# Kernel tuning notes

Measured on AMD Instinct MI355X. Metric: run time of the kernel, lower is better.

The kernel has to match this reference:

```python
import jax, jax.numpy as jnp
import numpy as np

N, M, IN_DIM, OUT_DIM = 32768, 8192, 256, 64


def setup_inputs() -> dict:
    key = jax.random.key(0)
    k1, k2, k3, k4 = jax.random.split(key, 4)
    H = jax.random.bernoulli(k1, 0.01, (N, M)).astype(jnp.float32)
    w = jax.random.uniform(k2, (M,), minval=0.5, maxval=1.5, dtype=jnp.float32)
    x = jax.random.normal(k3, (N, IN_DIM), dtype=jnp.float32)
    W_lin = jax.random.normal(k4, (IN_DIM, OUT_DIM), dtype=jnp.float32) * (1.0 / np.sqrt(IN_DIM))
    b_lin = jnp.zeros((OUT_DIM,), dtype=jnp.float32)
    return {"x": x, "H": H, "w": w, "W_lin": W_lin, "b_lin": b_lin}


def reference(x, H, w, W_lin, b_lin):
    # Theta = Dv^{-1/2} H diag(w) De^{-1} H^T Dv^{-1/2}; out = Theta @ (x W + b).
    # Applied right-to-left with O(N) diagonal broadcasts instead of materializing
    # the [N, N] operator -- identical math to the torch reference.
    De = jnp.clip(jnp.sum(H, axis=0), 1.0, None)                 # [M] edge degrees
    Dv = jnp.clip(jnp.sum(H * w[None, :], axis=1), 1e-6, None)   # [N] weighted node degrees
    dv_inv_sqrt = Dv ** -0.5                                     # [N]
    y = x @ W_lin + b_lin                                        # [N, out]
    t = H.T @ (dv_inv_sqrt[:, None] * y)                         # [M, out] gather to edges
    t = (w / De)[:, None] * t                                    # edge scaling W De^{-1}
    out = dv_inv_sqrt[:, None] * (H @ t)                         # [N, out] scatter back
    return out
```

## Files before the change

### kernel.cpp

```cpp
#include <hip/hip_runtime.h>

#define N_NODES 32768
#define M_EDGES 8192
#define IN_DIM  256
#define OUT_F   64

#define KC1 16
#define KC2 4

#define NB8 (N_NODES / 8)
#define MB8 (M_EDGES / 8)

typedef __attribute__((ext_vector_type(8))) short  bf16x8;
typedef __attribute__((ext_vector_type(4))) float  f32x4;

__device__ __forceinline__ unsigned short f2bf_rne(float f) {
    unsigned u = __float_as_uint(f);
    unsigned r = (u + 0x7FFFu + ((u >> 16) & 1u)) >> 16;
    return (unsigned short)r;
}
__device__ __forceinline__ float bf2f(unsigned short h) {
    return __uint_as_float(((unsigned)h) << 16);
}


__global__ __launch_bounds__(256) void k_pack(const float* __restrict__ H,
                                              unsigned char* __restrict__ Hb) {
    int lane = threadIdx.x & 63;
    int wv   = threadIdx.x >> 6;
    int n = blockIdx.x * 4 + wv;
    const float4* Hrow = (const float4*)(H + (size_t)n * M_EDGES);
    unsigned* hb_row = (unsigned*)(Hb + (size_t)n * MB8);

    for (int i0 = 0; i0 < 32; i0 += 4) {
        float4 h0 = Hrow[(i0 + 0) * 64 + lane];
        float4 h1 = Hrow[(i0 + 1) * 64 + lane];
        float4 h2 = Hrow[(i0 + 2) * 64 + lane];
        float4 h3 = Hrow[(i0 + 3) * 64 + lane];
        #define PACK1(hv, ii)                                                  \
        {                                                                      \
            unsigned long long B0 = __ballot(hv.x != 0.f);                     \
            unsigned long long B1 = __ballot(hv.y != 0.f);                     \
            unsigned long long B2 = __ballot(hv.z != 0.f);                     \
            unsigned long long B3 = __ballot(hv.w != 0.f);                     \
            unsigned long long s01 = (lane & 2) ? B1 : B0;                     \
            unsigned long long s23 = (lane & 2) ? B3 : B2;                     \
            unsigned long long ss  = (lane & 4) ? s23 : s01;                   \
            unsigned v = (lane & 1) ? (unsigned)(ss >> 32) : (unsigned)ss;     \
            if (lane < 8) hb_row[(ii) * 8 + lane] = v;                         \
        }
        PACK1(h0, i0 + 0)
        PACK1(h1, i0 + 1)
        PACK1(h2, i0 + 2)
        PACK1(h3, i0 + 3)
        #undef PACK1
    }
}

__global__ __launch_bounds__(256) void k_bt(const unsigned char* __restrict__ Hb,
                                            unsigned char* __restrict__ HTb) {
    int lane = threadIdx.x & 63;
    int wv   = threadIdx.x >> 6;
    int id = blockIdx.x * 4 + wv;
    int D  = id & 255;
    int n0 = (id >> 8) * 64;
    unsigned u = *(const unsigned*)(Hb + (size_t)(n0 + lane) * MB8 + D * 4);
    int mbase = ((D >> 3) << 8) + ((D & 1) << 7) + ((D >> 1) & 3);
    unsigned long long acc = 0;
    #pragma unroll
    for (int b = 0; b < 32; ++b) {
        unsigned long long bal = __ballot((u >> b) & 1u);
        acc = (lane == b) ? bal : acc;
    }
    if (lane < 32)
        *(unsigned long long*)(HTb + (size_t)(mbase + 4 * lane) * NB8 + (n0 >> 3)) = acc;
}

__global__ __launch_bounds__(256) void k_dv(const unsigned char* __restrict__ Hb,
                                            const float* __restrict__ w,
                                            float* __restrict__ Dv_raw) {
    int lane = threadIdx.x & 63;
    int wv   = threadIdx.x >> 6;
    int n = blockIdx.x * 4 + wv;
    const uint4* row = (const uint4*)(Hb + (size_t)n * MB8);
    uint4 u4 = row[lane];
    float dv = 0.f;
    #define DVD(uu, dd)                                                        \
    {                                                                          \
        unsigned u = (uu);                                                     \
        int D = lane * 4 + (dd);                                               \
        int base = ((D >> 3) << 8) + ((D & 1) << 7) + ((D >> 1) & 3);          \
        while (u) { int p = __ffs(u) - 1; dv += w[base + 4 * p]; u &= u - 1; } \
    }
    DVD(u4.x, 0) DVD(u4.y, 1) DVD(u4.z, 2) DVD(u4.w, 3)
    #undef DVD
    for (int off = 32; off; off >>= 1) dv += __shfl_down(dv, off, 64);
    if (lane == 0) Dv_raw[n] = dv;
}

__global__ __launch_bounds__(256) void k_lin(const float* __restrict__ x,
                                             const float* __restrict__ Wl,
                                             const float* __restrict__ b,
                                             float* __restrict__ y) {
    __shared__ float x_s[16 * IN_DIM];
    int tid = threadIdx.x;
    int n0 = blockIdx.x * 16;
    for (int i = tid; i < 16 * IN_DIM / 4; i += 256)
        ((float4*)x_s)[i] = ((const float4*)(x + (size_t)n0 * IN_DIM))[i];
    __syncthreads();
    int k = tid & 63;
    int rbase = tid >> 6;
    for (int pass = 0; pass < 4; ++pass) {
        int r = pass * 4 + rbase;
        float acc = b[k];
        const float* xr = x_s + r * IN_DIM;
        #pragma unroll 8
        for (int i = 0; i < IN_DIM; ++i)
            acc = fmaf(xr[i], Wl[i * OUT_F + k], acc);
        y[(size_t)(n0 + r) * OUT_F + k] = acc;
    }
}

__global__ __launch_bounds__(256) void k_zt(const float* __restrict__ y,
                                            const float* __restrict__ Dv_raw,
                                            unsigned short* __restrict__ zTh,
                                            unsigned short* __restrict__ zTl) {
    __shared__ unsigned short zh_s[64][264];
    __shared__ unsigned short zl_s[64][264];
    __shared__ float dvis_s[256];
    int t = threadIdx.x;
    int n0 = blockIdx.x * 256;
    dvis_s[t] = rsqrtf(fmaxf(Dv_raw[n0 + t], 1e-6f));
    __syncthreads();
    int c = t & 15, rp = t >> 4;
    for (int it = 0; it < 16; ++it) {
        int r = it * 16 + rp;
        float4 v = ((const float4*)(y + (size_t)(n0 + r) * OUT_F))[c];
        float dvs = dvis_s[r];
        float zv[4] = { v.x * dvs, v.y * dvs, v.z * dvs, v.w * dvs };
        #pragma unroll
        for (int j = 0; j < 4; ++j) {
            unsigned short hi = f2bf_rne(zv[j]);
            float lo = zv[j] - bf2f(hi);
            zh_s[4 * c + j][r] = hi;
            zl_s[4 * c + j][r] = f2bf_rne(lo);
        }
    }
    __syncthreads();
    int lane = t & 63, wv = t >> 6;
    for (int i = 0; i < 16; ++i) {
        int kk = wv * 16 + i;
        *(ushort4*)(zTh + (size_t)kk * N_NODES + n0 + lane * 4) =
            *(const ushort4*)&zh_s[kk][lane * 4];
        *(ushort4*)(zTl + (size_t)kk * N_NODES + n0 + lane * 4) =
            *(const ushort4*)&zl_s[kk][lane * 4];
    }
}

__global__ __launch_bounds__(256) void g1(const unsigned char* __restrict__ HTb,
                                          const unsigned short* __restrict__ zTh,
                                          const unsigned short* __restrict__ zTl,
                                          float* __restrict__ t_part) {
    __shared__ unsigned short lut[256][8];
    int t = threadIdx.x;
    #pragma unroll
    for (int j = 0; j < 8; ++j)
        lut[t][j] = ((t >> j) & 1) ? 0x3F80 : 0;
    __syncthreads();

    int lane = t & 63, wv = t >> 6;
    int l15 = lane & 15, l4 = lane >> 4;
    int m_base = blockIdx.x * 256 + wv * 64;
    int kc = blockIdx.y;
    int k_base = kc * (N_NODES / KC1);

    f32x4 acc[4][4];
    #pragma unroll
    for (int i = 0; i < 4; ++i)
        #pragma unroll
        for (int j = 0; j < 4; ++j) acc[i][j] = (f32x4){0.f, 0.f, 0.f, 0.f};

    const unsigned* arow[4];
    #pragma unroll
    for (int fr = 0; fr < 4; ++fr)
        arow[fr] = (const unsigned*)(HTb + (size_t)(m_base + fr * 16 + l15) * NB8);

    for (int kk = 0; kk < N_NODES / KC1; kk += 32) {
        int kd   = (k_base + kk) >> 5;
        int kidx = k_base + kk + l4 * 8;
        bf16x8 a[4], bh[4], bl[4];
        #pragma unroll
        for (int fr = 0; fr < 4; ++fr) {
            unsigned u  = arow[fr][kd];
            unsigned by = (u >> (l4 * 8)) & 255u;
            a[fr] = *(const bf16x8*)&lut[by][0];
        }
        #pragma unroll
        for (int fc = 0; fc < 4; ++fc) {
            bh[fc] = *(const bf16x8*)(zTh + (size_t)(fc * 16 + l15) * N_NODES + kidx);
            bl[fc] = *(const bf16x8*)(zTl + (size_t)(fc * 16 + l15) * N_NODES + kidx);
        }
        #pragma unroll
        for (int fr = 0; fr < 4; ++fr)
            #pragma unroll
            for (int fc = 0; fc < 4; ++fc) {
                acc[fr][fc] = __builtin_amdgcn_mfma_f32_16x16x32_bf16(a[fr], bh[fc], acc[fr][fc], 0, 0, 0);
                acc[fr][fc] = __builtin_amdgcn_mfma_f32_16x16x32_bf16(a[fr], bl[fc], acc[fr][fc], 0, 0, 0);
            }
    }
    float* dst = t_part + (size_t)kc * M_EDGES * OUT_F;
    #pragma unroll
    for (int fr = 0; fr < 4; ++fr)
        #pragma unroll
        for (int fc = 0; fc < 4; ++fc)
            #pragma unroll
            for (int r = 0; r < 4; ++r) {
                int row = m_base + fr * 16 + l4 * 4 + r;
                int col = fc * 16 + l15;
                dst[(size_t)row * OUT_F + col] = acc[fr][fc][r];
            }
}

__global__ __launch_bounds__(256) void k_tt(const float* __restrict__ t_part,
                                            const float* __restrict__ w,
                                            const unsigned char* __restrict__ HTb,
                                            unsigned short* __restrict__ tTh,
                                            unsigned short* __restrict__ tTl) {
    __shared__ unsigned short th_s[64][136];
    __shared__ unsigned short tl_s[64][136];
    __shared__ float de_s[128];
    int t = threadIdx.x;
    int m0 = blockIdx.x * 128;

    {
        int ml = t >> 1, hh = t & 1;
        const uint4* rp = (const uint4*)(HTb + (size_t)(m0 + ml) * NB8) + hh * 128;
        unsigned cnt = 0;
        #pragma unroll 4
        for (int i = 0; i < 128; ++i) {
            uint4 v = rp[i];
            cnt += (unsigned)(__popc(v.x) + __popc(v.y) + __popc(v.z) + __popc(v.w));
        }
        cnt += (unsigned)__shfl_xor((int)cnt, 1, 64);
        if (hh == 0) de_s[ml] = (float)cnt;
    }
    __syncthreads();

    int c = t & 15, rr = t >> 4;
    for (int it = 0; it < 8; ++it) {
        int ml = it * 16 + rr;
        float4 s = {0.f, 0.f, 0.f, 0.f};
        #pragma unroll
        for (int kc = 0; kc < KC1; ++kc) {
            float4 v = ((const float4*)(t_part + ((size_t)kc * M_EDGES + m0 + ml) * OUT_F))[c];
            s.x += v.x; s.y += v.y; s.z += v.z; s.w += v.w;
        }
        float sc = w[m0 + ml] / fmaxf(de_s[ml], 1.0f);
        float sv[4] = { s.x * sc, s.y * sc, s.z * sc, s.w * sc };
        #pragma unroll
        for (int j = 0; j < 4; ++j) {
            unsigned short hi = f2bf_rne(sv[j]);
            th_s[4 * c + j][ml] = hi;
            tl_s[4 * c + j][ml] = f2bf_rne(sv[j] - bf2f(hi));
        }
    }
    __syncthreads();
    for (int s = t; s < 64 * 128; s += 256) {
        int kk = s >> 7;
        int ml = s & 127;
        int m = m0 + ml;
        int R = ((m >> 8) << 8) + ((m & 3) << 6) + (((m >> 7) & 1) << 5)
              + (((m >> 5) & 3) << 3) + ((m >> 2) & 7);
        tTh[(size_t)kk * M_EDGES + R] = th_s[kk][ml];
        tTl[(size_t)kk * M_EDGES + R] = tl_s[kk][ml];
    }
}

__global__ __launch_bounds__(256) void g2(const unsigned char* __restrict__ Hb,
                                          const unsigned short* __restrict__ tTh,
                                          const unsigned short* __restrict__ tTl,
                                          float* __restrict__ out_part) {
    __shared__ unsigned short lut[256][8];
    int t = threadIdx.x;
    #pragma unroll
    for (int j = 0; j < 8; ++j)
        lut[t][j] = ((t >> j) & 1) ? 0x3F80 : 0;
    __syncthreads();

    int lane = t & 63, wv = t >> 6;
    int l15 = lane & 15, l4 = lane >> 4;
    int n_base = blockIdx.x * 256 + wv * 64;
    int h = blockIdx.y;
    int k_base = h * (M_EDGES / KC2);

    f32x4 acc[4][4];
    #pragma unroll
    for (int i = 0; i < 4; ++i)
        #pragma unroll
        for (int j = 0; j < 4; ++j) acc[i][j] = (f32x4){0.f, 0.f, 0.f, 0.f};

    const unsigned* arow[4];
    #pragma unroll
    for (int fr = 0; fr < 4; ++fr)
        arow[fr] = (const unsigned*)(Hb + (size_t)(n_base + fr * 16 + l15) * MB8);

    for (int kk = 0; kk < M_EDGES / KC2; kk += 32) {
        int kd   = (k_base + kk) >> 5;
        int kidx = k_base + kk + l4 * 8;
        bf16x8 a[4], bh[4], bl[4];
        #pragma unroll
        for (int fr = 0; fr < 4; ++fr) {
            unsigned u  = arow[fr][kd];
            unsigned by = (u >> (l4 * 8)) & 255u;
            a[fr] = *(const bf16x8*)&lut[by][0];
        }
        #pragma unroll
        for (int fc = 0; fc < 4; ++fc) {
            bh[fc] = *(const bf16x8*)(tTh + (size_t)(fc * 16 + l15) * M_EDGES + kidx);
            bl[fc] = *(const bf16x8*)(tTl + (size_t)(fc * 16 + l15) * M_EDGES + kidx);
        }
        #pragma unroll
        for (int fr = 0; fr < 4; ++fr)
            #pragma unroll
            for (int fc = 0; fc < 4; ++fc) {
                acc[fr][fc] = __builtin_amdgcn_mfma_f32_16x16x32_bf16(a[fr], bh[fc], acc[fr][fc], 0, 0, 0);
                acc[fr][fc] = __builtin_amdgcn_mfma_f32_16x16x32_bf16(a[fr], bl[fc], acc[fr][fc], 0, 0, 0);
            }
    }
    float* dst = out_part + (size_t)h * N_NODES * OUT_F;
    #pragma unroll
    for (int fr = 0; fr < 4; ++fr)
        #pragma unroll
        for (int fc = 0; fc < 4; ++fc)
            #pragma unroll
            for (int r = 0; r < 4; ++r) {
                int row = n_base + fr * 16 + l4 * 4 + r;
                int col = fc * 16 + l15;
                dst[(size_t)row * OUT_F + col] = acc[fr][fc][r];
            }
}

__global__ __launch_bounds__(256) void k_fin(const float* __restrict__ out_part,
                                             const float* __restrict__ Dv_raw,
                                             float* __restrict__ out) {
    int i4 = blockIdx.x * 256 + threadIdx.x;
    int n = i4 >> 4;
    float4 s = {0.f, 0.f, 0.f, 0.f};
    #pragma unroll
    for (int h = 0; h < KC2; ++h) {
        float4 v = ((const float4*)(out_part + (size_t)h * N_NODES * OUT_F))[i4];
        s.x += v.x; s.y += v.y; s.z += v.z; s.w += v.w;
    }
    float dvis = rsqrtf(fmaxf(Dv_raw[n], 1e-6f));
    float4 r = { s.x * dvis, s.y * dvis, s.z * dvis, s.w * dvis };
    ((float4*)out)[i4] = r;
}

extern "C" void kernel_launch(void* const* d_in, const int* in_sizes, int n_in,
                              void* d_out, int out_size, void* d_ws, size_t ws_size,
                              hipStream_t stream) {
    const float* x  = (const float*)d_in[0];
    const float* H  = (const float*)d_in[1];
    const float* w  = (const float*)d_in[2];
    const float* Wl = (const float*)d_in[3];
    const float* bl = (const float*)d_in[4];
    float* out = (float*)d_out;

    float* y      = (float*)d_ws;
    float* Dv_raw = y + (size_t)N_NODES * OUT_F;
    float* t_part = Dv_raw + N_NODES;
    float* o_part = t_part + (size_t)KC1 * M_EDGES * OUT_F;
    unsigned short* zTh = (unsigned short*)(o_part + (size_t)KC2 * N_NODES * OUT_F);
    unsigned short* zTl = zTh + (size_t)OUT_F * N_NODES;
    unsigned short* tTh = zTl + (size_t)OUT_F * N_NODES;
    unsigned short* tTl = tTh + (size_t)OUT_F * M_EDGES;
    unsigned char*  Hb  = (unsigned char*)(tTl + (size_t)OUT_F * M_EDGES);
    unsigned char*  HTb = Hb + (size_t)N_NODES * MB8;

    k_pack<<<dim3(N_NODES / 4), dim3(256), 0, stream>>>(H, Hb);
    k_bt  <<<dim3((N_NODES / 64) * (M_EDGES / 32) / 4), dim3(256), 0, stream>>>(Hb, HTb);
    k_dv  <<<dim3(N_NODES / 4), dim3(256), 0, stream>>>(Hb, w, Dv_raw);
    k_lin <<<dim3(N_NODES / 16), dim3(256), 0, stream>>>(x, Wl, bl, y);
    k_zt  <<<dim3(N_NODES / 256), dim3(256), 0, stream>>>(y, Dv_raw, zTh, zTl);
    g1    <<<dim3(M_EDGES / 256, KC1), dim3(256), 0, stream>>>(HTb, zTh, zTl, t_part);
    k_tt  <<<dim3(M_EDGES / 128), dim3(256), 0, stream>>>(t_part, w, HTb, tTh, tTl);
    g2    <<<dim3(N_NODES / 256, KC2), dim3(256), 0, stream>>>(Hb, tTh, tTl, o_part);
    k_fin <<<dim3(N_NODES * OUT_F / 4 / 256), dim3(256), 0, stream>>>(o_part, Dv_raw, out);
}
```

Baseline: 1.897 ms.

## Tile bit-transpose through LDS and shrink GEMM tiles with deeper split-K

k_bt now transposes a 512x512 bit tile per block. It stages ballot results in shared memory and writes 64-byte contiguous rows of HTb, replacing the scattered 8-byte stores. g1 and g2 halve the per-wave row tile from 64 to 32 and double the split-K factors (KC1 32, KC2 8), which gives four times as many blocks to fill the GPU. In exchange, each wave reuses the z/t B-operand loads less, and the partial-sum buffers and the reductions in k_tt and k_fin double in size.

Measured after the change: 2.141 ms. 12.9% more time.

```diff
diff --git a/kernel.cpp b/kernel.cpp
--- a/kernel.cpp
+++ b/kernel.cpp
@@ -5,8 +5,8 @@
 #define IN_DIM  256
 #define OUT_F   64
 
-#define KC1 16
-#define KC2 4
+#define KC1 32
+#define KC2 8
 
 #define NB8 (N_NODES / 8)
 #define MB8 (M_EDGES / 8)
@@ -59,21 +59,40 @@
 
 __global__ __launch_bounds__(256) void k_bt(const unsigned char* __restrict__ Hb,
                                             unsigned char* __restrict__ HTb) {
+    __shared__ unsigned long long ht[512][9];
     int lane = threadIdx.x & 63;
-    int wv   = threadIdx.x >> 6;
-    int id = blockIdx.x * 4 + wv;
-    int D  = id & 255;
-    int n0 = (id >> 8) * 64;
-    unsigned u = *(const unsigned*)(Hb + (size_t)(n0 + lane) * MB8 + D * 4);
-    int mbase = ((D >> 3) << 8) + ((D & 1) << 7) + ((D >> 1) & 3);
-    unsigned long long acc = 0;
-    #pragma unroll
-    for (int b = 0; b < 32; ++b) {
-        unsigned long long bal = __ballot((u >> b) & 1u);
-        acc = (lane == b) ? bal : acc;
-    }
-    if (lane < 32)
-        *(unsigned long long*)(HTb + (size_t)(mbase + 4 * lane) * NB8 + (n0 >> 3)) = acc;
+    int g    = threadIdx.x >> 6;
+    int n0 = blockIdx.x * 512;
+    int m0 = blockIdx.y * 512;
+
+    for (int c = 0; c < 2; ++c) {
+        int n = n0 + g * 128 + c * 64 + lane;
+        const uint4* src = (const uint4*)(Hb + (size_t)n * MB8 + (m0 >> 3));
+        uint4 q0 = src[0], q1 = src[1], q2 = src[2], q3 = src[3];
+        unsigned dws[16] = { q0.x, q0.y, q0.z, q0.w, q1.x, q1.y, q1.z, q1.w,
+                             q2.x, q2.y, q2.z, q2.w, q3.x, q3.y, q3.z, q3.w };
+        int slot = g * 2 + c;
+        #pragma unroll
+        for (int d = 0; d < 16; ++d) {
+            unsigned u = dws[d];
+            int mb = ((d >> 3) << 8) + ((d & 1) << 7) + ((d >> 1) & 3);
+            unsigned long long acc = 0;
+            #pragma unroll
+            for (int b = 0; b < 32; ++b) {
+                unsigned long long bal = __ballot((u >> b) & 1u);
+                acc = (lane == b) ? bal : acc;
+            }
+            if (lane < 32) ht[mb + 4 * lane][slot] = acc;
+        }
+    }
+    __syncthreads();
+    int t = threadIdx.x;
+    for (int i = 0; i < 16; ++i) {
+        int row  = (t >> 3) + 32 * i;
+        int slot = t & 7;
+        *(unsigned long long*)(HTb + (size_t)(m0 + row) * NB8 + (n0 >> 3) + slot * 8) =
+            ht[row][slot];
+    }
 }
 
 __global__ __launch_bounds__(256) void k_dv(const unsigned char* __restrict__ Hb,
@@ -170,27 +189,27 @@
 
     int lane = t & 63, wv = t >> 6;
     int l15 = lane & 15, l4 = lane >> 4;
-    int m_base = blockIdx.x * 256 + wv * 64;
+    int m_base = blockIdx.x * 128 + wv * 32;
     int kc = blockIdx.y;
     int k_base = kc * (N_NODES / KC1);
 
-    f32x4 acc[4][4];
-    #pragma unroll
-    for (int i = 0; i < 4; ++i)
+    f32x4 acc[2][4];
+    #pragma unroll
+    for (int i = 0; i < 2; ++i)
         #pragma unroll
         for (int j = 0; j < 4; ++j) acc[i][j] = (f32x4){0.f, 0.f, 0.f, 0.f};
 
-    const unsigned* arow[4];
-    #pragma unroll
-    for (int fr = 0; fr < 4; ++fr)
+    const unsigned* arow[2];
+    #pragma unroll
+    for (int fr = 0; fr < 2; ++fr)
         arow[fr] = (const unsigned*)(HTb + (size_t)(m_base + fr * 16 + l15) * NB8);
 
     for (int kk = 0; kk < N_NODES / KC1; kk += 32) {
         int kd   = (k_base + kk) >> 5;
         int kidx = k_base + kk + l4 * 8;
-        bf16x8 a[4], bh[4], bl[4];
-        #pragma unroll
-        for (int fr = 0; fr < 4; ++fr) {
+        bf16x8 a[2], bh[4], bl[4];
+        #pragma unroll
+        for (int fr = 0; fr < 2; ++fr) {
             unsigned u  = arow[fr][kd];
             unsigned by = (u >> (l4 * 8)) & 255u;
             a[fr] = *(const bf16x8*)&lut[by][0];
@@ -201,7 +220,7 @@
             bl[fc] = *(const bf16x8*)(zTl + (size_t)(fc * 16 + l15) * N_NODES + kidx);
         }
         #pragma unroll
-        for (int fr = 0; fr < 4; ++fr)
+        for (int fr = 0; fr < 2; ++fr)
             #pragma unroll
             for (int fc = 0; fc < 4; ++fc) {
                 acc[fr][fc] = __builtin_amdgcn_mfma_f32_16x16x32_bf16(a[fr], bh[fc], acc[fr][fc], 0, 0, 0);
@@ -210,7 +229,7 @@
     }
     float* dst = t_part + (size_t)kc * M_EDGES * OUT_F;
     #pragma unroll
-    for (int fr = 0; fr < 4; ++fr)
+    for (int fr = 0; fr < 2; ++fr)
         #pragma unroll
         for (int fc = 0; fc < 4; ++fc)
             #pragma unroll
@@ -289,27 +308,27 @@
 
     int lane = t & 63, wv = t >> 6;
     int l15 = lane & 15, l4 = lane >> 4;
-    int n_base = blockIdx.x * 256 + wv * 64;
+    int n_base = blockIdx.x * 128 + wv * 32;
     int h = blockIdx.y;
     int k_base = h * (M_EDGES / KC2);
 
-    f32x4 acc[4][4];
-    #pragma unroll
-    for (int i = 0; i < 4; ++i)
+    f32x4 acc[2][4];
+    #pragma unroll
+    for (int i = 0; i < 2; ++i)
         #pragma unroll
         for (int j = 0; j < 4; ++j) acc[i][j] = (f32x4){0.f, 0.f, 0.f, 0.f};
 
-    const unsigned* arow[4];
-    #pragma unroll
-    for (int fr = 0; fr < 4; ++fr)
+    const unsigned* arow[2];
+    #pragma unroll
+    for (int fr = 0; fr < 2; ++fr)
         arow[fr] = (const unsigned*)(Hb + (size_t)(n_base + fr * 16 + l15) * MB8);
 
     for (int kk = 0; kk < M_EDGES / KC2; kk += 32) {
         int kd   = (k_base + kk) >> 5;
         int kidx = k_base + kk + l4 * 8;
-        bf16x8 a[4], bh[4], bl[4];
-        #pragma unroll
-        for (int fr = 0; fr < 4; ++fr) {
+        bf16x8 a[2], bh[4], bl[4];
+        #pragma unroll
+        for (int fr = 0; fr < 2; ++fr) {
             unsigned u  = arow[fr][kd];
             unsigned by = (u >> (l4 * 8)) & 255u;
             a[fr] = *(const bf16x8*)&lut[by][0];
@@ -320,7 +339,7 @@
             bl[fc] = *(const bf16x8*)(tTl + (size_t)(fc * 16 + l15) * M_EDGES + kidx);
         }
         #pragma unroll
-        for (int fr = 0; fr < 4; ++fr)
+        for (int fr = 0; fr < 2; ++fr)
             #pragma unroll
             for (int fc = 0; fc < 4; ++fc) {
                 acc[fr][fc] = __builtin_amdgcn_mfma_f32_16x16x32_bf16(a[fr], bh[fc], acc[fr][fc], 0, 0, 0);
@@ -329,7 +348,7 @@
     }
     float* dst = out_part + (size_t)h * N_NODES * OUT_F;
     #pragma unroll
-    for (int fr = 0; fr < 4; ++fr)
+    for (int fr = 0; fr < 2; ++fr)
         #pragma unroll
         for (int fc = 0; fc < 4; ++fc)
             #pragma unroll
@@ -378,12 +397,12 @@
     unsigned char*  HTb = Hb + (size_t)N_NODES * MB8;
 
     k_pack<<<dim3(N_NODES / 4), dim3(256), 0, stream>>>(H, Hb);
-    k_bt  <<<dim3((N_NODES / 64) * (M_EDGES / 32) / 4), dim3(256), 0, stream>>>(Hb, HTb);
+    k_bt  <<<dim3(N_NODES / 512, M_EDGES / 512), dim3(256), 0, stream>>>(Hb, HTb);
     k_dv  <<<dim3(N_NODES / 4), dim3(256), 0, stream>>>(Hb, w, Dv_raw);
     k_lin <<<dim3(N_NODES / 16), dim3(256), 0, stream>>>(x, Wl, bl, y);
     k_zt  <<<dim3(N_NODES / 256), dim3(256), 0, stream>>>(y, Dv_raw, zTh, zTl);
-    g1    <<<dim3(M_EDGES / 256, KC1), dim3(256), 0, stream>>>(HTb, zTh, zTl, t_part);
+    g1    <<<dim3(M_EDGES / 128, KC1), dim3(256), 0, stream>>>(HTb, zTh, zTl, t_part);
     k_tt  <<<dim3(M_EDGES / 128), dim3(256), 0, stream>>>(t_part, w, HTb, tTh, tTl);
-    g2    <<<dim3(N_NODES / 256, KC2), dim3(256), 0, stream>>>(Hb, tTh, tTl, o_part);
+    g2    <<<dim3(N_NODES / 128, KC2), dim3(256), 0, stream>>>(Hb, tTh, tTl, o_part);
     k_fin <<<dim3(N_NODES * OUT_F / 4 / 256), dim3(256), 0, stream>>>(o_part, Dv_raw, out);
 }
```
